# Optimization experiments

Hardware: AMD Instinct MI355X
Metric: run time of the kernel (lower is better)

The kernel has to match this reference:

```python
import jax, jax.numpy as jnp
import numpy as np

B, H, E_DIM, V = 512, 2048, 1024, 50257


def setup_inputs() -> dict:
    key = jax.random.key(0)
    ks = jax.random.split(key, 10)
    s_e = 1.0 / np.sqrt(E_DIM)
    s_h = 1.0 / np.sqrt(H)
    return {
        "inp": jax.random.randint(ks[0], (B,), 0, V),
        "h_0": jax.random.normal(ks[1], (B, H), jnp.float32) * 0.1,
        "c_0": jax.random.normal(ks[2], (B, H), jnp.float32) * 0.1,
        "E": jax.random.normal(ks[3], (V, E_DIM), jnp.float32),
        "Wx": jax.random.normal(ks[4], (4, H, E_DIM), jnp.float32) * s_e,
        "bx": jax.random.normal(ks[5], (4, H), jnp.float32) * s_e,
        "Wh": jax.random.normal(ks[6], (4, H, H), jnp.float32) * s_h,
        "bh": jax.random.normal(ks[7], (4, H), jnp.float32) * s_h,
        "Wd": jax.random.normal(ks[8], (V, H), jnp.float32) * s_h,
        "bd": jax.random.normal(ks[9], (V,), jnp.float32) * s_h,
    }


def reference(inp, h_0, c_0, E, Wx, bx, Wh, bh, Wd, bd):
    # Embedding lookup: [B, E_DIM]
    x = E[inp]
    # Two fused GEMMs for all 4 gates (gate order: f, i, o, c): [B, 4, H]
    gates = (jnp.einsum('be,ghe->bgh', x, Wx) + bx[None]
             + jnp.einsum('bh,gkh->bgk', h_0, Wh) + bh[None])
    f_g = jax.nn.sigmoid(gates[:, 0])
    i_g = jax.nn.sigmoid(gates[:, 1])
    o_g = jax.nn.sigmoid(gates[:, 2])
    c_tilda = jnp.tanh(gates[:, 3])
    cx = f_g * c_0 + i_g * c_tilda
    hx = o_g * jnp.tanh(cx)
    out = hx @ Wd.T + bd  # [B, V]
    return out, hx, cx
```

## Files before the change

### kernel.cpp

```cpp
#include <hip/hip_runtime.h>
#include <hip/hip_bf16.h>

using bf16x8 = __attribute__((ext_vector_type(8))) short;
using f32x4  = __attribute__((ext_vector_type(4))) float;

#define DEVI __device__ __forceinline__

DEVI unsigned short bf16r(float f)
{
    return __builtin_bit_cast(unsigned short, __float2bfloat16(f));
}

DEVI bf16x8 cvt8(const f32x4 a, const f32x4 b)
{
    bf16x8 r;
#pragma unroll
    for (int j = 0; j < 4; ++j) {
        r[j]     = (short)bf16r(a[j]);
        r[4 + j] = (short)bf16r(b[j]);
    }
    return r;
}

__global__ __launch_bounds__(256) void k_gather(const float* __restrict__ E,
                                                const int* __restrict__ inp,
                                                unsigned short* __restrict__ x)
{
    const int b = blockIdx.x;
    const long r = inp[b];
    const f32x4 v = ((const f32x4*)(E + r * 1024L))[threadIdx.x];
    ushort4 o;
    o.x = bf16r(v[0]); o.y = bf16r(v[1]); o.z = bf16r(v[2]); o.w = bf16r(v[3]);
    ((ushort4*)(x + (long)b * 1024L))[threadIdx.x] = o;
}

__global__ __launch_bounds__(256) void k_cvt(const float* __restrict__ in,
                                             unsigned short* __restrict__ out)
{
    const long i = (blockIdx.x * 256L + threadIdx.x) * 8;
    const f32x4 a = *(const f32x4*)(in + i);
    const f32x4 b = *(const f32x4*)(in + i + 4);
    *(bf16x8*)(out + i) = cvt8(a, b);
}


DEVI bf16x8 lds_frag(const char* lds, int row, int j)
{
    return *(const bf16x8*)(lds + row * 128 + ((j ^ (row & 7)) << 4));
}

DEVI void mfma_tile(const char* sA, const char* sB, int l, int wr, int wc,
                    f32x4 (&acc)[4][4])
{
#pragma unroll
    for (int ks = 0; ks < 2; ++ks) {
        bf16x8 af[4], bq[4];
#pragma unroll
        for (int m = 0; m < 4; ++m)
            af[m] = lds_frag(sA, wr * 64 + m * 16 + (l & 15), ks * 4 + (l >> 4));
#pragma unroll
        for (int n = 0; n < 4; ++n)
            bq[n] = lds_frag(sB, wc * 64 + n * 16 + (l & 15), ks * 4 + (l >> 4));
#pragma unroll
        for (int m = 0; m < 4; ++m)
#pragma unroll
            for (int n = 0; n < 4; ++n)
                acc[m][n] = __builtin_amdgcn_mfma_f32_16x16x32_bf16(
                    af[m], bq[n], acc[m][n], 0, 0, 0);
    }
}

template <bool CLAMP>
DEVI void gemm_core(const unsigned short* __restrict__ A, long lda, long arow0,
                    const float* __restrict__ B, long ldb, long brow0, long bmax,
                    int ntiles, long kbase, int t, char* sA, char* sB,
                    f32x4 (&acc)[4][4])
{
    const int l = t & 63;
    const int wr = (t >> 7) & 1, wc = (t >> 6) & 1;

    const unsigned short* ap[4];
#pragma unroll
    for (int i = 0; i < 4; ++i) {
        const int g = i * 256 + t, row = g >> 3, js = g & 7;
        ap[i] = A + (arow0 + row) * lda + kbase + (long)((js ^ (row & 7)) * 8);
    }
    const float* bp[4];
#pragma unroll
    for (int i = 0; i < 4; ++i) {
        const int g = i * 256 + t, row = g >> 3, j = g & 7;
        long br = brow0 + row;
        if (CLAMP) br = (br < bmax) ? br : (bmax - 1);
        bp[i] = B + br * ldb + kbase + (long)(j * 8);
    }

    f32x4 br0[4], br1[4];
#pragma unroll
    for (int i = 0; i < 4; ++i) {
        br0[i] = *(const f32x4*)bp[i];
        br1[i] = *(const f32x4*)(bp[i] + 4);
        bp[i] += 64;
    }

    for (int ti = 0; ti < ntiles; ++ti) {
        __syncthreads();
#pragma unroll
        for (int i = 0; i < 4; ++i)
            __builtin_amdgcn_global_load_lds(
                (const __attribute__((address_space(1))) void*)(ap[i]),
                (__attribute__((address_space(3))) void*)(sA + (i * 256 + t) * 16),
                16, 0, 0);
#pragma unroll
        for (int i = 0; i < 4; ++i) {
            const int g = i * 256 + t, row = g >> 3, j = g & 7;
            *(bf16x8*)(sB + row * 128 + ((j ^ (row & 7)) << 4)) = cvt8(br0[i], br1[i]);
        }
        __syncthreads();
#pragma unroll
        for (int i = 0; i < 4; ++i) ap[i] += 64;
        if (ti + 1 < ntiles) {
#pragma unroll
            for (int i = 0; i < 4; ++i) {
                br0[i] = *(const f32x4*)bp[i];
                br1[i] = *(const f32x4*)(bp[i] + 4);
                bp[i] += 64;
            }
        }
        mfma_tile(sA, sB, l, wr, wc, acc);
    }
}

__global__ __launch_bounds__(256, 3) void k_gates(
    const unsigned short* __restrict__ xb, const float* __restrict__ Wx,
    const unsigned short* __restrict__ h0b, const float* __restrict__ Wh,
    float* __restrict__ g0, float* __restrict__ g1, float* __restrict__ g2)
{
    __shared__ __align__(16) char sA[128 * 128];
    __shared__ __align__(16) char sB[128 * 128];
    const int t = threadIdx.x;
    const int bid = blockIdx.x;
    const int xcd = bid & 7, slot = bid >> 3;
    const int L = xcd * 96 + slot;
    const int mtile = L & 3;
    const int rest = L >> 2;
    const int ntile = rest & 63;
    const int z = rest >> 6;

    const unsigned short* A; const float* B; long lda, ldb, kbase; float* C;
    if (z == 0)      { A = xb;  lda = 1024; B = Wx; ldb = 1024; kbase = 0;    C = g0; }
    else if (z == 1) { A = h0b; lda = 2048; B = Wh; ldb = 2048; kbase = 0;    C = g1; }
    else             { A = h0b; lda = 2048; B = Wh; ldb = 2048; kbase = 1024; C = g2; }

    f32x4 acc[4][4] = {};
    gemm_core<false>(A, lda, (long)mtile * 128, B, ldb, (long)ntile * 128,
                     1L << 40, 16, kbase, t, sA, sB, acc);

    const int l = t & 63;
    const int wr = (t >> 7) & 1, wc = (t >> 6) & 1;
    const int lc = l & 15, r4 = (l >> 4) * 4;
#pragma unroll
    for (int n = 0; n < 4; ++n) {
        const long col = (long)ntile * 128 + wc * 64 + n * 16 + lc;
#pragma unroll
        for (int m = 0; m < 4; ++m) {
            const long row = (long)mtile * 128 + wr * 64 + m * 16 + r4;
#pragma unroll
            for (int r = 0; r < 4; ++r)
                C[(row + r) * 8192 + col] = acc[m][n][r];
        }
    }
}

__global__ __launch_bounds__(256, 3) void k_dec(
    const unsigned short* __restrict__ hxb, const float* __restrict__ Wd,
    const float* __restrict__ bd, float* __restrict__ out)
{
    __shared__ __align__(16) char sA[128 * 128];
    __shared__ __align__(16) char sB[128 * 128];
    const int t = threadIdx.x;
    const int bid = blockIdx.x;
    const int xcd = bid & 7, slot = bid >> 3;
    const int L = xcd * 196 + (xcd < 4 ? xcd : 4) + slot;
    const int mtile = L & 3;
    const int ntile = L >> 2;
    const long N = 50257;

    f32x4 acc[4][4] = {};
    gemm_core<true>(hxb, 2048, (long)mtile * 128, Wd, 2048, (long)ntile * 128,
                    N, 32, 0, t, sA, sB, acc);

    const int l = t & 63;
    const int wr = (t >> 7) & 1, wc = (t >> 6) & 1;
    const int lc = l & 15, r4 = (l >> 4) * 4;
#pragma unroll
    for (int n = 0; n < 4; ++n) {
        const long col = (long)ntile * 128 + wc * 64 + n * 16 + lc;
        if (col >= N) continue;
        const float bias = bd[col];
#pragma unroll
        for (int m = 0; m < 4; ++m) {
            const long row = (long)mtile * 128 + wr * 64 + m * 16 + r4;
#pragma unroll
            for (int r = 0; r < 4; ++r)
                out[(row + r) * N + col] = acc[m][n][r] + bias;
        }
    }
}

__global__ __launch_bounds__(256) void k_lstm(
    const float* __restrict__ g0, const float* __restrict__ g1,
    const float* __restrict__ g2, const float* __restrict__ bx,
    const float* __restrict__ bh, const float* __restrict__ c0,
    float* __restrict__ hx, float* __restrict__ cx,
    unsigned short* __restrict__ hxb)
{
    const int i = blockIdx.x * 256 + threadIdx.x;
    const int b = i >> 9;
    const int hc = (i & 511) << 2;
    const long base = (long)b * 8192;

    f32x4 g[4];
#pragma unroll
    for (int gi = 0; gi < 4; ++gi) {
        const long off = base + gi * 2048 + hc;
        const int boff = gi * 2048 + hc;
        g[gi] = *(const f32x4*)(g0 + off);
        g[gi] += *(const f32x4*)(g1 + off);
        g[gi] += *(const f32x4*)(g2 + off);
        g[gi] += *(const f32x4*)(bx + boff);
        g[gi] += *(const f32x4*)(bh + boff);
    }
    const f32x4 c0v = *(const f32x4*)(c0 + (long)b * 2048 + hc);

    f32x4 cv, hv;
    ushort4 hb;
#pragma unroll
    for (int j = 0; j < 4; ++j) {
        const float fg = 1.f / (1.f + __expf(-g[0][j]));
        const float ig = 1.f / (1.f + __expf(-g[1][j]));
        const float og = 1.f / (1.f + __expf(-g[2][j]));
        const float e2 = __expf(2.f * g[3][j]);
        const float ct = 1.f - 2.f / (e2 + 1.f);
        const float c  = fg * c0v[j] + ig * ct;
        const float e2c = __expf(2.f * c);
        const float th  = 1.f - 2.f / (e2c + 1.f);
        cv[j] = c;
        hv[j] = og * th;
    }
    hb.x = bf16r(hv[0]); hb.y = bf16r(hv[1]); hb.z = bf16r(hv[2]); hb.w = bf16r(hv[3]);

    const long o = (long)b * 2048 + hc;
    *(f32x4*)(cx + o) = cv;
    *(f32x4*)(hx + o) = hv;
    *(ushort4*)(hxb + o) = hb;
}

extern "C" void kernel_launch(void* const* d_in, const int* in_sizes, int n_in,
                              void* d_out, int out_size, void* d_ws, size_t ws_size,
                              hipStream_t stream)
{
    const int*   inp = (const int*)d_in[0];
    const float* h0  = (const float*)d_in[1];
    const float* c0  = (const float*)d_in[2];
    const float* E   = (const float*)d_in[3];
    const float* Wx  = (const float*)d_in[4];
    const float* bx  = (const float*)d_in[5];
    const float* Wh  = (const float*)d_in[6];
    const float* bh  = (const float*)d_in[7];
    const float* Wd  = (const float*)d_in[8];
    const float* bd  = (const float*)d_in[9];

    float* out = (float*)d_out;
    float* hx  = out + 512L * 50257L;
    float* cx  = hx + 512L * 2048L;

    unsigned short* xb  = (unsigned short*)out;
    float* g0 = out + (1L << 20);
    float* g1 = out + (5L << 20);
    float* g2 = out + (9L << 20);
    unsigned short* h0b = (unsigned short*)(out + (13L << 20));
    unsigned short* hxb = (unsigned short*)d_ws;

    k_gather<<<512, 256, 0, stream>>>(E, inp, xb);
    k_cvt<<<512, 256, 0, stream>>>(h0, h0b);

    k_gates<<<768, 256, 0, stream>>>(xb, Wx, h0b, Wh, g0, g1, g2);

    k_lstm<<<1024, 256, 0, stream>>>(g0, g1, g2, bx, bh, c0, hx, cx, hxb);

    k_dec<<<1572, 256, 0, stream>>>(hxb, Wd, bd, out);
}
```

Measured before the change: 296.1 us.

## Double-buffer LDS tiles in GEMM core to overlap loads with MFMA

The shared GEMM core now uses two A/B shared-memory buffers and ping-pongs between them. It issues the async A copy and the bf16 conversion of B for the next tile while MFMAs run on the current tile, which cuts the barrier count per tile from two to one. The aim is to hide global-load and LDS-write latency behind compute. In exchange, LDS per block doubles to 64 KB and launch bounds drop to 2 blocks per CU, and it keeps two register sets of prefetched B data, so occupancy falls.

```diff
diff --git a/kernel.cpp b/kernel.cpp
--- a/kernel.cpp
+++ b/kernel.cpp
@@ -73,7 +73,8 @@
 template <bool CLAMP>
 DEVI void gemm_core(const unsigned short* __restrict__ A, long lda, long arow0,
                     const float* __restrict__ B, long ldb, long brow0, long bmax,
-                    int ntiles, long kbase, int t, char* sA, char* sB,
+                    int ntiles, long kbase, int t,
+                    char* sA0, char* sB0, char* sA1, char* sB1,
                     f32x4 (&acc)[4][4])
 {
     const int l = t & 63;
@@ -86,57 +87,75 @@
         ap[i] = A + (arow0 + row) * lda + kbase + (long)((js ^ (row & 7)) * 8);
     }
     const float* bp[4];
+    int swz[4];
 #pragma unroll
     for (int i = 0; i < 4; ++i) {
         const int g = i * 256 + t, row = g >> 3, j = g & 7;
         long br = brow0 + row;
         if (CLAMP) br = (br < bmax) ? br : (bmax - 1);
         bp[i] = B + br * ldb + kbase + (long)(j * 8);
-    }
-
-    f32x4 br0[4], br1[4];
-#pragma unroll
-    for (int i = 0; i < 4; ++i) {
-        br0[i] = *(const f32x4*)bp[i];
-        br1[i] = *(const f32x4*)(bp[i] + 4);
-        bp[i] += 64;
-    }
-
-    for (int ti = 0; ti < ntiles; ++ti) {
+        swz[i] = row * 128 + ((j ^ (row & 7)) << 4);
+    }
+
+    f32x4 b0lo[4], b0hi[4], b1lo[4], b1hi[4];
+
+#define LOADB(lo, hi)                                                          \
+    do {                                                                       \
+        _Pragma("unroll") for (int i = 0; i < 4; ++i) {                        \
+            lo[i] = *(const f32x4*)bp[i];                                      \
+            hi[i] = *(const f32x4*)(bp[i] + 4);                                \
+            bp[i] += 64;                                                       \
+        }                                                                      \
+    } while (0)
+#define DMA_A(buf)                                                             \
+    do {                                                                       \
+        _Pragma("unroll") for (int i = 0; i < 4; ++i) {                        \
+            __builtin_amdgcn_global_load_lds(                                  \
+                (const __attribute__((address_space(1))) void*)(ap[i]),        \
+                (__attribute__((address_space(3))) void*)((buf) +              \
+                                                          (i * 256 + t) * 16), \
+                16, 0, 0);                                                     \
+            ap[i] += 64;                                                       \
+        }                                                                      \
+    } while (0)
+#define WRITEB(buf, lo, hi)                                                    \
+    do {                                                                       \
+        _Pragma("unroll") for (int i = 0; i < 4; ++i)                          \
+            *(bf16x8*)((buf) + swz[i]) = cvt8(lo[i], hi[i]);                   \
+    } while (0)
+
+    LOADB(b0lo, b0hi);
+    DMA_A(sA0);
+    WRITEB(sB0, b0lo, b0hi);
+    LOADB(b1lo, b1hi);
+    __syncthreads();
+
+    for (int ti = 0; ti < ntiles; ti += 2) {
+        DMA_A(sA1);
+        if (ti + 2 < ntiles) LOADB(b0lo, b0hi);
+        WRITEB(sB1, b1lo, b1hi);
+        mfma_tile(sA0, sB0, l, wr, wc, acc);
         __syncthreads();
-#pragma unroll
-        for (int i = 0; i < 4; ++i)
-            __builtin_amdgcn_global_load_lds(
-                (const __attribute__((address_space(1))) void*)(ap[i]),
-                (__attribute__((address_space(3))) void*)(sA + (i * 256 + t) * 16),
-                16, 0, 0);
-#pragma unroll
-        for (int i = 0; i < 4; ++i) {
-            const int g = i * 256 + t, row = g >> 3, j = g & 7;
-            *(bf16x8*)(sB + row * 128 + ((j ^ (row & 7)) << 4)) = cvt8(br0[i], br1[i]);
+        if (ti + 2 < ntiles) {
+            DMA_A(sA0);
+            if (ti + 3 < ntiles) LOADB(b1lo, b1hi);
+            WRITEB(sB0, b0lo, b0hi);
         }
+        mfma_tile(sA1, sB1, l, wr, wc, acc);
         __syncthreads();
-#pragma unroll
-        for (int i = 0; i < 4; ++i) ap[i] += 64;
-        if (ti + 1 < ntiles) {
-#pragma unroll
-            for (int i = 0; i < 4; ++i) {
-                br0[i] = *(const f32x4*)bp[i];
-                br1[i] = *(const f32x4*)(bp[i] + 4);
-                bp[i] += 64;
-            }
-        }
-        mfma_tile(sA, sB, l, wr, wc, acc);
-    }
-}
-
-__global__ __launch_bounds__(256, 3) void k_gates(
+    }
+#undef LOADB
+#undef DMA_A
+#undef WRITEB
+}
+
+__global__ __launch_bounds__(256, 2) void k_gates(
     const unsigned short* __restrict__ xb, const float* __restrict__ Wx,
     const unsigned short* __restrict__ h0b, const float* __restrict__ Wh,
     float* __restrict__ g0, float* __restrict__ g1, float* __restrict__ g2)
 {
-    __shared__ __align__(16) char sA[128 * 128];
-    __shared__ __align__(16) char sB[128 * 128];
+    __shared__ __align__(16) char sA0[128 * 128], sB0[128 * 128];
+    __shared__ __align__(16) char sA1[128 * 128], sB1[128 * 128];
     const int t = threadIdx.x;
     const int bid = blockIdx.x;
     const int xcd = bid & 7, slot = bid >> 3;
@@ -153,7 +172,7 @@
 
     f32x4 acc[4][4] = {};
     gemm_core<false>(A, lda, (long)mtile * 128, B, ldb, (long)ntile * 128,
-                     1L << 40, 16, kbase, t, sA, sB, acc);
+                     1L << 40, 16, kbase, t, sA0, sB0, sA1, sB1, acc);
 
     const int l = t & 63;
     const int wr = (t >> 7) & 1, wc = (t >> 6) & 1;
@@ -171,12 +190,12 @@
     }
 }
 
-__global__ __launch_bounds__(256, 3) void k_dec(
+__global__ __launch_bounds__(256, 2) void k_dec(
     const unsigned short* __restrict__ hxb, const float* __restrict__ Wd,
     const float* __restrict__ bd, float* __restrict__ out)
 {
-    __shared__ __align__(16) char sA[128 * 128];
-    __shared__ __align__(16) char sB[128 * 128];
+    __shared__ __align__(16) char sA0[128 * 128], sB0[128 * 128];
+    __shared__ __align__(16) char sA1[128 * 128], sB1[128 * 128];
     const int t = threadIdx.x;
     const int bid = blockIdx.x;
     const int xcd = bid & 7, slot = bid >> 3;
@@ -187,7 +206,7 @@
 
     f32x4 acc[4][4] = {};
     gemm_core<true>(hxb, 2048, (long)mtile * 128, Wd, 2048, (long)ntile * 128,
-                    N, 32, 0, t, sA, sB, acc);
+                    N, 32, 0, t, sA0, sB0, sA1, sB1, acc);
 
     const int l = t & 63;
     const int wr = (t >> 7) & 1, wc = (t >> 6) & 1;
```

Measured after the change: 285.6 us. 3.5% less time.

## Pre-convert weight matrices to bf16 and load both GEMM operands via global_load_lds

Applied to the files above, without the earlier changes.

The fp32 weights Wx, Wh and Wd are now converted to bf16 in separate passes into workspace buffers. The Wd conversion is folded into the gates kernel as extra blocks that run alongside the gate GEMM tiles. Both GEMMs then stream bf16 B tiles straight into LDS with global_load_lds instead of a register load, convert and LDS store. This removes in-loop conversion and halves the operand bytes the GEMM loops read. In exchange it adds a full fp32 read plus bf16 write pass over about 100M Wd elements every call, and drops the register prefetch of B.

```diff
diff --git a/kernel.cpp b/kernel.cpp
--- a/kernel.cpp
+++ b/kernel.cpp
@@ -34,8 +34,8 @@
     ((ushort4*)(x + (long)b * 1024L))[threadIdx.x] = o;
 }
 
-__global__ __launch_bounds__(256) void k_cvt(const float* __restrict__ in,
-                                             unsigned short* __restrict__ out)
+__global__ __launch_bounds__(256) void k_cvtn(const float* __restrict__ in,
+                                              unsigned short* __restrict__ out)
 {
     const long i = (blockIdx.x * 256L + threadIdx.x) * 8;
     const f32x4 a = *(const f32x4*)(in + i);
@@ -72,73 +72,70 @@
 
 template <bool CLAMP>
 DEVI void gemm_core(const unsigned short* __restrict__ A, long lda, long arow0,
-                    const float* __restrict__ B, long ldb, long brow0, long bmax,
-                    int ntiles, long kbase, int t, char* sA, char* sB,
-                    f32x4 (&acc)[4][4])
+                    const unsigned short* __restrict__ B, long ldb, long brow0,
+                    long bmax, int ntiles, long kbase, int t,
+                    char* sA, char* sB, f32x4 (&acc)[4][4])
 {
     const int l = t & 63;
     const int wr = (t >> 7) & 1, wc = (t >> 6) & 1;
 
     const unsigned short* ap[4];
+    const unsigned short* bp[4];
 #pragma unroll
     for (int i = 0; i < 4; ++i) {
         const int g = i * 256 + t, row = g >> 3, js = g & 7;
-        ap[i] = A + (arow0 + row) * lda + kbase + (long)((js ^ (row & 7)) * 8);
-    }
-    const float* bp[4];
-#pragma unroll
-    for (int i = 0; i < 4; ++i) {
-        const int g = i * 256 + t, row = g >> 3, j = g & 7;
+        const long ko = kbase + (long)((js ^ (row & 7)) * 8);
+        ap[i] = A + (arow0 + row) * lda + ko;
         long br = brow0 + row;
         if (CLAMP) br = (br < bmax) ? br : (bmax - 1);
-        bp[i] = B + br * ldb + kbase + (long)(j * 8);
-    }
-
-    f32x4 br0[4], br1[4];
-#pragma unroll
-    for (int i = 0; i < 4; ++i) {
-        br0[i] = *(const f32x4*)bp[i];
-        br1[i] = *(const f32x4*)(bp[i] + 4);
-        bp[i] += 64;
+        bp[i] = B + br * ldb + ko;
     }
 
     for (int ti = 0; ti < ntiles; ++ti) {
         __syncthreads();
 #pragma unroll
-        for (int i = 0; i < 4; ++i)
+        for (int i = 0; i < 4; ++i) {
             __builtin_amdgcn_global_load_lds(
                 (const __attribute__((address_space(1))) void*)(ap[i]),
                 (__attribute__((address_space(3))) void*)(sA + (i * 256 + t) * 16),
                 16, 0, 0);
+            ap[i] += 64;
+        }
 #pragma unroll
         for (int i = 0; i < 4; ++i) {
-            const int g = i * 256 + t, row = g >> 3, j = g & 7;
-            *(bf16x8*)(sB + row * 128 + ((j ^ (row & 7)) << 4)) = cvt8(br0[i], br1[i]);
+            __builtin_amdgcn_global_load_lds(
+                (const __attribute__((address_space(1))) void*)(bp[i]),
+                (__attribute__((address_space(3))) void*)(sB + (i * 256 + t) * 16),
+                16, 0, 0);
+            bp[i] += 64;
         }
         __syncthreads();
-#pragma unroll
-        for (int i = 0; i < 4; ++i) ap[i] += 64;
-        if (ti + 1 < ntiles) {
-#pragma unroll
-            for (int i = 0; i < 4; ++i) {
-                br0[i] = *(const f32x4*)bp[i];
-                br1[i] = *(const f32x4*)(bp[i] + 4);
-                bp[i] += 64;
-            }
-        }
         mfma_tile(sA, sB, l, wr, wc, acc);
     }
 }
 
-__global__ __launch_bounds__(256, 3) void k_gates(
-    const unsigned short* __restrict__ xb, const float* __restrict__ Wx,
-    const unsigned short* __restrict__ h0b, const float* __restrict__ Wh,
-    float* __restrict__ g0, float* __restrict__ g1, float* __restrict__ g2)
-{
-    __shared__ __align__(16) char sA[128 * 128];
-    __shared__ __align__(16) char sB[128 * 128];
+__global__ __launch_bounds__(256, 3) void k_gates_cvt(
+    const unsigned short* __restrict__ xb, const unsigned short* __restrict__ Wxb,
+    const unsigned short* __restrict__ h0b, const unsigned short* __restrict__ Whb,
+    float* __restrict__ g0, float* __restrict__ g1, float* __restrict__ g2,
+    const float* __restrict__ Wd, unsigned short* __restrict__ Wdb)
+{
+    __shared__ __align__(16) char sA[16384];
+    __shared__ __align__(16) char sB[16384];
     const int t = threadIdx.x;
     const int bid = blockIdx.x;
+
+    if (bid >= 768) {
+        const long stride = 1264L * 256 * 8;
+        long i = ((bid - 768) * 256L + t) * 8;
+        for (; i < 102926336L; i += stride) {
+            const f32x4 a = *(const f32x4*)(Wd + i);
+            const f32x4 b = *(const f32x4*)(Wd + i + 4);
+            *(bf16x8*)(Wdb + i) = cvt8(a, b);
+        }
+        return;
+    }
+
     const int xcd = bid & 7, slot = bid >> 3;
     const int L = xcd * 96 + slot;
     const int mtile = L & 3;
@@ -146,10 +143,10 @@
     const int ntile = rest & 63;
     const int z = rest >> 6;
 
-    const unsigned short* A; const float* B; long lda, ldb, kbase; float* C;
-    if (z == 0)      { A = xb;  lda = 1024; B = Wx; ldb = 1024; kbase = 0;    C = g0; }
-    else if (z == 1) { A = h0b; lda = 2048; B = Wh; ldb = 2048; kbase = 0;    C = g1; }
-    else             { A = h0b; lda = 2048; B = Wh; ldb = 2048; kbase = 1024; C = g2; }
+    const unsigned short *A, *B; long lda, ldb, kbase; float* C;
+    if (z == 0)      { A = xb;  lda = 1024; B = Wxb; ldb = 1024; kbase = 0;    C = g0; }
+    else if (z == 1) { A = h0b; lda = 2048; B = Whb; ldb = 2048; kbase = 0;    C = g1; }
+    else             { A = h0b; lda = 2048; B = Whb; ldb = 2048; kbase = 1024; C = g2; }
 
     f32x4 acc[4][4] = {};
     gemm_core<false>(A, lda, (long)mtile * 128, B, ldb, (long)ntile * 128,
@@ -172,11 +169,11 @@
 }
 
 __global__ __launch_bounds__(256, 3) void k_dec(
-    const unsigned short* __restrict__ hxb, const float* __restrict__ Wd,
+    const unsigned short* __restrict__ hxb, const unsigned short* __restrict__ Wdb,
     const float* __restrict__ bd, float* __restrict__ out)
 {
-    __shared__ __align__(16) char sA[128 * 128];
-    __shared__ __align__(16) char sB[128 * 128];
+    __shared__ __align__(16) char sA[16384];
+    __shared__ __align__(16) char sB[16384];
     const int t = threadIdx.x;
     const int bid = blockIdx.x;
     const int xcd = bid & 7, slot = bid >> 3;
@@ -186,7 +183,7 @@
     const long N = 50257;
 
     f32x4 acc[4][4] = {};
-    gemm_core<true>(hxb, 2048, (long)mtile * 128, Wd, 2048, (long)ntile * 128,
+    gemm_core<true>(hxb, 2048, (long)mtile * 128, Wdb, 2048, (long)ntile * 128,
                     N, 32, 0, t, sA, sB, acc);
 
     const int l = t & 63;
@@ -279,14 +276,20 @@
     float* g1 = out + (5L << 20);
     float* g2 = out + (9L << 20);
     unsigned short* h0b = (unsigned short*)(out + (13L << 20));
-    unsigned short* hxb = (unsigned short*)d_ws;
+    char* ws = (char*)d_ws;
+    unsigned short* hxb = (unsigned short*)ws;
+    unsigned short* Wdb = (unsigned short*)(ws + (4L << 20));
+    unsigned short* Wxb = (unsigned short*)(ws + (216L << 20));
+    unsigned short* Whb = (unsigned short*)(ws + (236L << 20));
 
     k_gather<<<512, 256, 0, stream>>>(E, inp, xb);
-    k_cvt<<<512, 256, 0, stream>>>(h0, h0b);
-
-    k_gates<<<768, 256, 0, stream>>>(xb, Wx, h0b, Wh, g0, g1, g2);
+    k_cvtn<<<512, 256, 0, stream>>>(h0, h0b);
+    k_cvtn<<<4096, 256, 0, stream>>>(Wx, Wxb);
+    k_cvtn<<<8192, 256, 0, stream>>>(Wh, Whb);
+
+    k_gates_cvt<<<2032, 256, 0, stream>>>(xb, Wxb, h0b, Whb, g0, g1, g2, Wd, Wdb);
 
     k_lstm<<<1024, 256, 0, stream>>>(g0, g1, g2, bx, bh, c0, hx, cx, hxb);
 
-    k_dec<<<1572, 256, 0, stream>>>(hxb, Wd, bd, out);
-}
+    k_dec<<<1572, 256, 0, stream>>>(hxb, Wdb, bd, out);
+}
```

Result: slower. 349.9 us (+18.2%).
